# Optimization experiments

Measured on AMD Instinct MI355X. Metric: run time of the kernel, lower is better.

## Reference

```python
import jax, jax.numpy as jnp
import numpy as np
import math

B, S, IN_DIM = 4, 2048, 256
ATT_DIM, NUM_HEADS, TOP_K = 128, 4, 32


def _linear_params(key, out_dim, in_dim):
    kw, kb = jax.random.split(key)
    bound = 1.0 / math.sqrt(in_dim)
    w = jax.random.uniform(kw, (out_dim, in_dim), jnp.float32, -bound, bound)
    b = jax.random.uniform(kb, (out_dim,), jnp.float32, -bound, bound)
    return w, b


def setup_inputs() -> dict:
    key = jax.random.key(0)
    keys = jax.random.split(key, 16)
    x = jax.random.normal(keys[0], (B, S, IN_DIM), jnp.float32)
    tp_w, tp_b = _linear_params(keys[1], ATT_DIM, IN_DIM)
    sp_w, sp_b = _linear_params(keys[2], ATT_DIM, IN_DIM)
    ta_qw, ta_qb = _linear_params(keys[3], ATT_DIM, ATT_DIM)
    ta_kw, ta_kb = _linear_params(keys[4], ATT_DIM, ATT_DIM)
    ta_vw, ta_vb = _linear_params(keys[5], ATT_DIM, ATT_DIM)
    ta_ow, ta_ob = _linear_params(keys[6], ATT_DIM, ATT_DIM)
    sa_qw, sa_qb = _linear_params(keys[7], ATT_DIM, ATT_DIM)
    sa_kw, sa_kb = _linear_params(keys[8], ATT_DIM, ATT_DIM)
    sa_vw, sa_vb = _linear_params(keys[9], ATT_DIM, ATT_DIM)
    sa_ow, sa_ob = _linear_params(keys[10], ATT_DIM, ATT_DIM)
    gate_w, gate_b = _linear_params(keys[11], ATT_DIM, 2 * ATT_DIM)
    fus_w, fus_b = _linear_params(keys[12], ATT_DIM, 2 * ATT_DIM)
    return dict(x=x, tp_w=tp_w, tp_b=tp_b, sp_w=sp_w, sp_b=sp_b,
                ta_qw=ta_qw, ta_qb=ta_qb, ta_kw=ta_kw, ta_kb=ta_kb,
                ta_vw=ta_vw, ta_vb=ta_vb, ta_ow=ta_ow, ta_ob=ta_ob,
                sa_qw=sa_qw, sa_qb=sa_qb, sa_kw=sa_kw, sa_kb=sa_kb,
                sa_vw=sa_vw, sa_vb=sa_vb, sa_ow=sa_ow, sa_ob=sa_ob,
                gate_w=gate_w, gate_b=gate_b, fus_w=fus_w, fus_b=fus_b)


def _lin(x, w, b):
    return x @ w.T + b


def _sparse_topk_attention(x, qw, qb, kw, kb, vw, vb, ow, ob):
    # x: [B, S, E]; dropout is identity in eval mode
    b, s, e = x.shape
    h, d = NUM_HEADS, e // NUM_HEADS
    q = _lin(x, qw, qb).reshape(b, s, h, d).transpose(0, 2, 1, 3)  # [B,H,S,D]
    k = _lin(x, kw, kb).reshape(b, s, h, d).transpose(0, 2, 1, 3)
    v = _lin(x, vw, vb).reshape(b, s, h, d).transpose(0, 2, 1, 3)
    scores = jnp.einsum('bhqd,bhkd->bhqk', q, k) / math.sqrt(d)  # [B,H,S,S]
    kk = min(TOP_K, s)
    top_scores, top_idx = jax.lax.top_k(scores, kk)  # [B,H,S,K]
    soft = jax.nn.softmax(top_scores, axis=-1)
    # scatter softmaxed top-k weights into a zero [B,H,S,S] matrix (faithful to source)
    bi = jnp.arange(b)[:, None, None, None]
    hi = jnp.arange(h)[None, :, None, None]
    si = jnp.arange(s)[None, None, :, None]
    sparse = jnp.zeros_like(scores).at[bi, hi, si, top_idx].set(soft)
    out = jnp.einsum('bhqk,bhkd->bhqd', sparse, v)
    out = out.transpose(0, 2, 1, 3).reshape(b, s, e)
    return _lin(out, ow, ob)


def reference(x, tp_w, tp_b, sp_w, sp_b,
              ta_qw, ta_qb, ta_kw, ta_kb, ta_vw, ta_vb, ta_ow, ta_ob,
              sa_qw, sa_qb, sa_kw, sa_kb, sa_vw, sa_vb, sa_ow, sa_ob,
              gate_w, gate_b, fus_w, fus_b):
    temporal = _lin(x, tp_w, tp_b)
    temporal = _sparse_topk_attention(temporal, ta_qw, ta_qb, ta_kw, ta_kb,
                                      ta_vw, ta_vb, ta_ow, ta_ob)
    semantic = _lin(x, sp_w, sp_b)
    semantic = _sparse_topk_attention(semantic, sa_qw, sa_qb, sa_kw, sa_kb,
                                      sa_vw, sa_vb, sa_ow, sa_ob)
    concat = jnp.concatenate([temporal, semantic], axis=-1)  # [B,S,2A]
    gate = jax.nn.sigmoid(_lin(concat, gate_w, gate_b))
    fused = _lin(concat, fus_w, fus_b) * gate
    return fused
```

## Files before the change

### kernel.cpp

```cpp
#include <hip/hip_runtime.h>
#include <math.h>

#define B_   4
#define S_   2048
#define AD   128
#define NH   4
#define HD   32
#define TK   32
#define SEG  1048576
#define CAP  192

#define OFF_PROJ 0
#define OFF_Q    (1 * SEG)
#define OFF_K    (2 * SEG)
#define OFF_V    (3 * SEG)
#define OFF_ATT  (4 * SEG)
#define OFF_T    (5 * SEG)
#define OFF_SB   (6 * SEG)
#define OFF_CAT  (7 * SEG)

__device__ float g_ws[9 * SEG];
__device__ float g_sc[8 * S_ * S_];

__device__ __forceinline__ unsigned f2key(float s) {
    unsigned u = __float_as_uint(s);
    return (u & 0x80000000u) ? ~u : (u | 0x80000000u);
}
__device__ __forceinline__ float key2f(unsigned k) {
    unsigned u = (k & 0x80000000u) ? (k & 0x7FFFFFFFu) : ~k;
    return __uint_as_float(u);
}

template <int KD>
__global__ __launch_bounds__(256)
void lin_kernel(const float* __restrict__ Xext, int xoff,
                const float* __restrict__ W, const float* __restrict__ Bv,
                int yoff)
{
    const float* X = Xext ? Xext : (const float*)(g_ws + xoff);
    float* Y = g_ws + yoff;
    __shared__ float Xs[32][68];
    __shared__ float Ws[32][68];
    const int bm = blockIdx.x * 64;
    const int bn = blockIdx.y * 64;
    const int t  = threadIdx.x;
    const int tx = t & 15, ty = t >> 4;
    const int sr = t >> 3, sc4 = t & 7;
    float acc[4][4] = {};
    for (int kk = 0; kk < KD; kk += 32) {
        #pragma unroll
        for (int it = 0; it < 2; ++it) {
            int rr = sr + it * 32;
            float4 xa = *(const float4*)(X + (size_t)(bm + rr) * KD + kk + sc4 * 4);
            float4 wa = *(const float4*)(W + (size_t)(bn + rr) * KD + kk + sc4 * 4);
            Xs[sc4*4+0][rr] = xa.x; Xs[sc4*4+1][rr] = xa.y;
            Xs[sc4*4+2][rr] = xa.z; Xs[sc4*4+3][rr] = xa.w;
            Ws[sc4*4+0][rr] = wa.x; Ws[sc4*4+1][rr] = wa.y;
            Ws[sc4*4+2][rr] = wa.z; Ws[sc4*4+3][rr] = wa.w;
        }
        __syncthreads();
        #pragma unroll
        for (int kc = 0; kc < 32; ++kc) {
            float4 a4 = *(const float4*)&Xs[kc][ty * 4];
            float4 b4 = *(const float4*)&Ws[kc][tx * 4];
            float a[4] = {a4.x, a4.y, a4.z, a4.w};
            float bb[4] = {b4.x, b4.y, b4.z, b4.w};
            #pragma unroll
            for (int i = 0; i < 4; ++i)
                #pragma unroll
                for (int j = 0; j < 4; ++j)
                    acc[i][j] = fmaf(a[i], bb[j], acc[i][j]);
        }
        __syncthreads();
    }
    #pragma unroll
    for (int i = 0; i < 4; ++i) {
        int row = bm + ty * 4 + i;
        int col = bn + tx * 4;
        float4 o;
        o.x = acc[i][0] + Bv[col + 0]; o.y = acc[i][1] + Bv[col + 1];
        o.z = acc[i][2] + Bv[col + 2]; o.w = acc[i][3] + Bv[col + 3];
        *(float4*)(Y + (size_t)row * AD + col) = o;
    }
}

template <int KD>
__global__ __launch_bounds__(256)
void lin3_kernel(int xoff,
                 const float* __restrict__ W0, const float* __restrict__ B0, int y0,
                 const float* __restrict__ W1, const float* __restrict__ B1, int y1,
                 const float* __restrict__ W2, const float* __restrict__ B2, int y2)
{
    const int z = blockIdx.z;
    const float* X = (const float*)(g_ws + xoff);
    const float* W = (z == 0) ? W0 : (z == 1) ? W1 : W2;
    const float* Bv = (z == 0) ? B0 : (z == 1) ? B1 : B2;
    float* Y = g_ws + ((z == 0) ? y0 : (z == 1) ? y1 : y2);
    __shared__ float Xs[32][68];
    __shared__ float Ws[32][68];
    const int bm = blockIdx.x * 64;
    const int bn = blockIdx.y * 64;
    const int t  = threadIdx.x;
    const int tx = t & 15, ty = t >> 4;
    const int sr = t >> 3, sc4 = t & 7;
    float acc[4][4] = {};
    for (int kk = 0; kk < KD; kk += 32) {
        #pragma unroll
        for (int it = 0; it < 2; ++it) {
            int rr = sr + it * 32;
            float4 xa = *(const float4*)(X + (size_t)(bm + rr) * KD + kk + sc4 * 4);
            float4 wa = *(const float4*)(W + (size_t)(bn + rr) * KD + kk + sc4 * 4);
            Xs[sc4*4+0][rr] = xa.x; Xs[sc4*4+1][rr] = xa.y;
            Xs[sc4*4+2][rr] = xa.z; Xs[sc4*4+3][rr] = xa.w;
            Ws[sc4*4+0][rr] = wa.x; Ws[sc4*4+1][rr] = wa.y;
            Ws[sc4*4+2][rr] = wa.z; Ws[sc4*4+3][rr] = wa.w;
        }
        __syncthreads();
        #pragma unroll
        for (int kc = 0; kc < 32; ++kc) {
            float4 a4 = *(const float4*)&Xs[kc][ty * 4];
            float4 b4 = *(const float4*)&Ws[kc][tx * 4];
            float a[4] = {a4.x, a4.y, a4.z, a4.w};
            float bb[4] = {b4.x, b4.y, b4.z, b4.w};
            #pragma unroll
            for (int i = 0; i < 4; ++i)
                #pragma unroll
                for (int j = 0; j < 4; ++j)
                    acc[i][j] = fmaf(a[i], bb[j], acc[i][j]);
        }
        __syncthreads();
    }
    #pragma unroll
    for (int i = 0; i < 4; ++i) {
        int row = bm + ty * 4 + i;
        int col = bn + tx * 4;
        float4 o;
        o.x = acc[i][0] + Bv[col + 0]; o.y = acc[i][1] + Bv[col + 1];
        o.z = acc[i][2] + Bv[col + 2]; o.w = acc[i][3] + Bv[col + 3];
        *(float4*)(Y + (size_t)row * AD + col) = o;
    }
}

__global__ __launch_bounds__(256)
void score_kernel(int qoff, int koff, int chunk)
{
    const int zh = blockIdx.z;
    const int hh = chunk * 8 + zh, b = hh >> 2, h = hh & 3;
    const float* Qb = g_ws + qoff + (size_t)b * S_ * AD + h * HD;
    const float* Kb = g_ws + koff + (size_t)b * S_ * AD + h * HD;
    float* Sc = g_sc + (size_t)zh * S_ * S_;
    __shared__ float Qs[32][68];
    __shared__ float Ks[32][68];
    const int t = threadIdx.x, tx = t & 15, ty = t >> 4;
    const int sr = t >> 3, sc4 = t & 7;
    const int q0 = blockIdx.y * 64, k0 = blockIdx.x * 64;
    #pragma unroll
    for (int it = 0; it < 2; ++it) {
        int rr = sr + it * 32;
        float4 qa = *(const float4*)(Qb + (size_t)(q0 + rr) * AD + sc4 * 4);
        float4 ka = *(const float4*)(Kb + (size_t)(k0 + rr) * AD + sc4 * 4);
        Qs[sc4*4+0][rr] = qa.x; Qs[sc4*4+1][rr] = qa.y;
        Qs[sc4*4+2][rr] = qa.z; Qs[sc4*4+3][rr] = qa.w;
        Ks[sc4*4+0][rr] = ka.x; Ks[sc4*4+1][rr] = ka.y;
        Ks[sc4*4+2][rr] = ka.z; Ks[sc4*4+3][rr] = ka.w;
    }
    __syncthreads();
    float acc[4][4] = {};
    #pragma unroll
    for (int kc = 0; kc < 32; ++kc) {
        float4 a4 = *(const float4*)&Qs[kc][ty * 4];
        float4 b4 = *(const float4*)&Ks[kc][tx * 4];
        float a[4] = {a4.x, a4.y, a4.z, a4.w};
        float bb[4] = {b4.x, b4.y, b4.z, b4.w};
        #pragma unroll
        for (int i = 0; i < 4; ++i)
            #pragma unroll
            for (int j = 0; j < 4; ++j)
                acc[i][j] = fmaf(a[i], bb[j], acc[i][j]);
    }
    const float scale = 0.17677669529663688f;
    #pragma unroll
    for (int i = 0; i < 4; ++i) {
        float4 o;
        o.x = acc[i][0] * scale; o.y = acc[i][1] * scale;
        o.z = acc[i][2] * scale; o.w = acc[i][3] * scale;
        *(float4*)(Sc + (size_t)(q0 + ty * 4 + i) * S_ + k0 + tx * 4) = o;
    }
}

__global__ __launch_bounds__(256)
void topk_kernel(int voff, int ooff, int chunk)
{
    const float* V = g_ws + voff;
    float* O = g_ws + ooff;

    __shared__ unsigned long long sve[4][CAP];
    __shared__ float    wsel[4][32];
    __shared__ unsigned jsel[4][32];

    const int wid  = threadIdx.x >> 6;
    const int lane = threadIdx.x & 63;
    const int gr   = blockIdx.x * 4 + wid;
    const int zh   = gr >> 11, q = gr & 2047;
    const int hh   = chunk * 8 + zh;
    const int b    = hh >> 2,  h = hh & 3;

    unsigned long long* sv = sve[wid];
    float*    wp = wsel[wid];
    unsigned* jp = jsel[wid];

    const float* Srow  = g_sc + (size_t)zh * S_ * S_ + (size_t)q * S_;
    const float* vbase = V + (size_t)b * S_ * AD + h * HD;

    float4 s4[8];
    #pragma unroll
    for (int i = 0; i < 8; ++i) s4[i] = ((const float4*)Srow)[i * 64 + lane];
    unsigned keys[32];
    unsigned lmax = 0u;
    #pragma unroll
    for (int i = 0; i < 8; ++i) {
        unsigned k0 = f2key(s4[i].x), k1 = f2key(s4[i].y);
        unsigned k2 = f2key(s4[i].z), k3 = f2key(s4[i].w);
        keys[i * 4 + 0] = k0; keys[i * 4 + 1] = k1;
        keys[i * 4 + 2] = k2; keys[i * 4 + 3] = k3;
        unsigned m01 = (k0 > k1) ? k0 : k1;
        unsigned m23 = (k2 > k3) ? k2 : k3;
        unsigned m = (m01 > m23) ? m01 : m23;
        lmax = (m > lmax) ? m : lmax;
    }

    unsigned bs = lmax;
    #pragma unroll
    for (int k = 2; k <= 64; k <<= 1) {
        #pragma unroll
        for (int j = k >> 1; j > 0; j >>= 1) {
            unsigned o = (unsigned)__shfl_xor((int)bs, j);
            bool up = ((lane & k) == 0);
            bool lower = ((lane & j) == 0);
            bs = (up == lower) ? (bs < o ? bs : o) : (bs > o ? bs : o);
        }
    }
    const unsigned thr  = (unsigned)__shfl((int)bs, 32);
    const unsigned mkey = (unsigned)__shfl((int)bs, 63);
    const float Mf = key2f(mkey);

    int base = 0;
    const unsigned long long lt = (1ull << lane) - 1ull;
    #pragma unroll
    for (int t = 0; t < 32; ++t) {
        bool pred = keys[t] >= thr;
        unsigned long long m = __ballot(pred);
        int slot = base + __popcll(m & lt);
        if (pred && slot < CAP) {
            unsigned jidx = (unsigned)((t >> 2) * 256 + lane * 4 + (t & 3));
            sv[slot] = ((unsigned long long)keys[t] << 32) | (unsigned)(2047 - jidx);
        }
        base += __popcll(m);
    }
    const int S = base;
    asm volatile("s_waitcnt lgkmcnt(0)" ::: "memory");

    if (S <= 64) {
        unsigned long long pi = (lane < S) ? sv[lane] : 0ull;
        int rank = 0;
        for (int jx = 0; jx < S; ++jx)
            rank += (sv[jx] > pi) ? 1 : 0;
        float e = 0.f; unsigned ji = 0;
        if (lane < S && rank < TK) {
            float val = key2f((unsigned)(pi >> 32));
            e = __expf(val - Mf);
            ji = 2047u - (unsigned)(pi & 0xFFFFFFFFull);
        }
        float esum = e;
        #pragma unroll
        for (int off = 1; off < 64; off <<= 1) esum += __shfl_xor(esum, off);
        if (lane < S && rank < TK) { wp[rank] = e / esum; jp[rank] = ji; }
    } else if (S <= CAP) {
        unsigned long long pi[3]; int rk[3]; float ee[3]; unsigned jj[3];
        float esum = 0.f;
        #pragma unroll
        for (int u = 0; u < 3; ++u) {
            int i = lane + u * 64;
            pi[u] = (i < S) ? sv[i] : 0ull;
            rk[u] = 0; ee[u] = 0.f; jj[u] = 0;
        }
        for (int jx = 0; jx < S; ++jx) {
            unsigned long long pj = sv[jx];
            #pragma unroll
            for (int u = 0; u < 3; ++u)
                rk[u] += (pj > pi[u]) ? 1 : 0;
        }
        #pragma unroll
        for (int u = 0; u < 3; ++u) {
            int i = lane + u * 64;
            if (i < S && rk[u] < TK) {
                float val = key2f((unsigned)(pi[u] >> 32));
                ee[u] = __expf(val - Mf);
                jj[u] = 2047u - (unsigned)(pi[u] & 0xFFFFFFFFull);
                esum += ee[u];
            }
        }
        #pragma unroll
        for (int off = 1; off < 64; off <<= 1) esum += __shfl_xor(esum, off);
        #pragma unroll
        for (int u = 0; u < 3; ++u) {
            int i = lane + u * 64;
            if (i < S && rk[u] < TK) { wp[rk[u]] = ee[u] / esum; jp[rk[u]] = jj[u]; }
        }
    } else {
        unsigned consumed = 0u;
        for (int i = 0; i < TK; ++i) {
            unsigned bk = 0u; unsigned gj = 0xFFFFFFFFu;
            #pragma unroll
            for (int t = 0; t < 32; ++t) {
                if (((consumed >> t) & 1u) == 0u) {
                    unsigned kk = keys[t];
                    unsigned j = (unsigned)((t >> 2) * 256 + lane * 4 + (t & 3));
                    if (kk > bk || (kk == bk && j < gj)) { bk = kk; gj = j; }
                }
            }
            #pragma unroll
            for (int off = 1; off < 64; off <<= 1) {
                unsigned ok = (unsigned)__shfl_xor((int)bk, off);
                unsigned oj = (unsigned)__shfl_xor((int)gj, off);
                if (ok > bk || (ok == bk && oj < gj)) { bk = ok; gj = oj; }
            }
            if (((gj >> 2) & 63u) == (unsigned)lane && gj != 0xFFFFFFFFu) {
                int t = ((int)gj >> 8) * 4 + ((int)gj & 3);
                consumed |= (1u << t);
            }
            if (lane == 0) { wp[i] = key2f(bk); jp[i] = gj; }
        }
        asm volatile("s_waitcnt lgkmcnt(0)" ::: "memory");
        float v = (lane < TK) ? wp[lane] : 0.f;
        float e = (lane < TK) ? __expf(v - Mf) : 0.f;
        float esum = e;
        #pragma unroll
        for (int off = 1; off < 64; off <<= 1) esum += __shfl_xor(esum, off);
        if (lane < TK) wp[lane] = e / esum;
    }
    asm volatile("s_waitcnt lgkmcnt(0)" ::: "memory");

    float oacc = 0.f;
    const int dd = lane & 31, half = lane >> 5;
    #pragma unroll
    for (int u2 = 0; u2 < 16; ++u2) {
        int i = half * 16 + u2;
        oacc = fmaf(wp[i], vbase[(size_t)jp[i] * AD + dd], oacc);
    }
    oacc += __shfl_down(oacc, 32);
    if (lane < HD) O[((size_t)b * S_ + q) * AD + h * HD + lane] = oacc;
}

__global__ __launch_bounds__(256)
void concat_kernel()
{
    int i = blockIdx.x * 256 + threadIdx.x;
    int row = i >> 8, c = i & 255;
    float v = (c < AD) ? g_ws[OFF_T + row * AD + c]
                       : g_ws[OFF_SB + row * AD + (c - AD)];
    g_ws[OFF_CAT + i] = v;
}

__global__ __launch_bounds__(256)
void fuse_kernel(float* __restrict__ out)
{
    int i = blockIdx.x * 256 + threadIdx.x;
    float g = g_ws[OFF_Q + i];
    float f = g_ws[OFF_K + i];
    out[i] = f / (1.0f + expf(-g));
}

extern "C" void kernel_launch(void* const* d_in, const int* in_sizes, int n_in,
                              void* d_out, int out_size, void* d_ws, size_t ws_size,
                              hipStream_t stream)
{
    (void)in_sizes; (void)n_in; (void)d_ws; (void)ws_size; (void)out_size;
    const float* x      = (const float*)d_in[0];
    const float* tp_w   = (const float*)d_in[1];
    const float* tp_b   = (const float*)d_in[2];
    const float* sp_w   = (const float*)d_in[3];
    const float* sp_b   = (const float*)d_in[4];
    const float* gate_w = (const float*)d_in[21];
    const float* gate_b = (const float*)d_in[22];
    const float* fus_w  = (const float*)d_in[23];
    const float* fus_b  = (const float*)d_in[24];

    dim3 gl(128, 2);
    for (int br = 0; br < 2; ++br) {
        const float* pw = br ? sp_w : tp_w;
        const float* pb = br ? sp_b : tp_b;
        int base = 5 + br * 8;
        const float* qw = (const float*)d_in[base + 0];
        const float* qb = (const float*)d_in[base + 1];
        const float* kw = (const float*)d_in[base + 2];
        const float* kb = (const float*)d_in[base + 3];
        const float* vw = (const float*)d_in[base + 4];
        const float* vb = (const float*)d_in[base + 5];
        const float* ow = (const float*)d_in[base + 6];
        const float* ob = (const float*)d_in[base + 7];

        lin_kernel<256><<<gl, 256, 0, stream>>>(x, 0, pw, pb, OFF_PROJ);
        lin3_kernel<128><<<dim3(128, 2, 3), 256, 0, stream>>>(
            OFF_PROJ, qw, qb, OFF_Q, kw, kb, OFF_K, vw, vb, OFF_V);
        for (int chunk = 0; chunk < 2; ++chunk) {
            score_kernel<<<dim3(32, 32, 8), 256, 0, stream>>>(OFF_Q, OFF_K, chunk);
            topk_kernel<<<4096, 256, 0, stream>>>(OFF_V, OFF_ATT, chunk);
        }
        lin_kernel<128><<<gl, 256, 0, stream>>>(nullptr, OFF_ATT, ow, ob,
                                                br ? OFF_SB : OFF_T);
    }
    concat_kernel<<<8192, 256, 0, stream>>>();
    lin3_kernel<256><<<dim3(128, 2, 2), 256, 0, stream>>>(
        OFF_CAT, gate_w, gate_b, OFF_Q, fus_w, fus_b, OFF_K,
        (const float*)nullptr, (const float*)nullptr, 0);
    fuse_kernel<<<4096, 256, 0, stream>>>((float*)d_out);
}
```

Measured before the change: 373.3 us.

## Store 16-bit score keys and recompute exact scores for top-k candidates

The score kernel now writes only the upper 16 bits of the order-preserving key instead of full fp32 scores. That halves the size of the score matrix, so all 16 heads fit in one buffer and the per-chunk launch loop can be dropped. The top-k kernel filters candidates with the truncated keys, then recomputes exact fp32 dot products from Q and K for those candidates before ranking and the softmax. This trades score-matrix memory traffic for extra gathered K reads. The fallback path, used when there are too many candidates, recomputes all 2048 scores per row.

```diff
diff --git a/kernel.cpp b/kernel.cpp
--- a/kernel.cpp
+++ b/kernel.cpp
@@ -20,7 +20,7 @@
 #define OFF_CAT  (7 * SEG)
 
 __device__ float g_ws[9 * SEG];
-__device__ float g_sc[8 * S_ * S_];
+__device__ unsigned short g_sp[16 * S_ * S_];
 
 __device__ __forceinline__ unsigned f2key(float s) {
     unsigned u = __float_as_uint(s);
@@ -142,13 +142,12 @@
 }
 
 __global__ __launch_bounds__(256)
-void score_kernel(int qoff, int koff, int chunk)
-{
-    const int zh = blockIdx.z;
-    const int hh = chunk * 8 + zh, b = hh >> 2, h = hh & 3;
+void score_kernel(int qoff, int koff)
+{
+    const int hh = blockIdx.z, b = hh >> 2, h = hh & 3;
     const float* Qb = g_ws + qoff + (size_t)b * S_ * AD + h * HD;
     const float* Kb = g_ws + koff + (size_t)b * S_ * AD + h * HD;
-    float* Sc = g_sc + (size_t)zh * S_ * S_;
+    unsigned short* Sc = g_sp + (size_t)hh * S_ * S_;
     __shared__ float Qs[32][68];
     __shared__ float Ks[32][68];
     const int t = threadIdx.x, tx = t & 15, ty = t >> 4;
@@ -181,19 +180,19 @@
     const float scale = 0.17677669529663688f;
     #pragma unroll
     for (int i = 0; i < 4; ++i) {
-        float4 o;
-        o.x = acc[i][0] * scale; o.y = acc[i][1] * scale;
-        o.z = acc[i][2] * scale; o.w = acc[i][3] * scale;
-        *(float4*)(Sc + (size_t)(q0 + ty * 4 + i) * S_ + k0 + tx * 4) = o;
-    }
-}
-
-__global__ __launch_bounds__(256)
-void topk_kernel(int voff, int ooff, int chunk)
-{
-    const float* V = g_ws + voff;
-    float* O = g_ws + ooff;
-
+        ushort4 o;
+        o.x = (unsigned short)(f2key(acc[i][0] * scale) >> 16);
+        o.y = (unsigned short)(f2key(acc[i][1] * scale) >> 16);
+        o.z = (unsigned short)(f2key(acc[i][2] * scale) >> 16);
+        o.w = (unsigned short)(f2key(acc[i][3] * scale) >> 16);
+        *(ushort4*)(Sc + (size_t)(q0 + ty * 4 + i) * S_ + k0 + tx * 4) = o;
+    }
+}
+
+__global__ __launch_bounds__(256)
+void topk_kernel(int qoff, int koff, int voff, int ooff)
+{
+    __shared__ unsigned cnd[4][CAP];
     __shared__ unsigned long long sve[4][CAP];
     __shared__ float    wsel[4][32];
     __shared__ unsigned jsel[4][32];
@@ -201,31 +200,32 @@
     const int wid  = threadIdx.x >> 6;
     const int lane = threadIdx.x & 63;
     const int gr   = blockIdx.x * 4 + wid;
-    const int zh   = gr >> 11, q = gr & 2047;
-    const int hh   = chunk * 8 + zh;
+    const int hh   = gr >> 11, q = gr & 2047;
     const int b    = hh >> 2,  h = hh & 3;
 
+    unsigned* cp = cnd[wid];
     unsigned long long* sv = sve[wid];
     float*    wp = wsel[wid];
     unsigned* jp = jsel[wid];
 
-    const float* Srow  = g_sc + (size_t)zh * S_ * S_ + (size_t)q * S_;
-    const float* vbase = V + (size_t)b * S_ * AD + h * HD;
-
-    float4 s4[8];
-    #pragma unroll
-    for (int i = 0; i < 8; ++i) s4[i] = ((const float4*)Srow)[i * 64 + lane];
-    unsigned keys[32];
+    const unsigned short* Prow = g_sp + (size_t)hh * S_ * S_ + (size_t)q * S_;
+    const float* qrow  = g_ws + qoff + ((size_t)b * S_ + q) * AD + h * HD;
+    const float* kbase = g_ws + koff + (size_t)b * S_ * AD + h * HD;
+    const float* vbase = g_ws + voff + (size_t)b * S_ * AD + h * HD;
+    float* O = g_ws + ooff;
+    const float scale = 0.17677669529663688f;
+
+    unsigned pwv[16];
     unsigned lmax = 0u;
     #pragma unroll
-    for (int i = 0; i < 8; ++i) {
-        unsigned k0 = f2key(s4[i].x), k1 = f2key(s4[i].y);
-        unsigned k2 = f2key(s4[i].z), k3 = f2key(s4[i].w);
-        keys[i * 4 + 0] = k0; keys[i * 4 + 1] = k1;
-        keys[i * 4 + 2] = k2; keys[i * 4 + 3] = k3;
-        unsigned m01 = (k0 > k1) ? k0 : k1;
-        unsigned m23 = (k2 > k3) ? k2 : k3;
-        unsigned m = (m01 > m23) ? m01 : m23;
+    for (int i = 0; i < 4; ++i) {
+        uint4 u = ((const uint4*)Prow)[i * 64 + lane];
+        pwv[i*4+0] = u.x; pwv[i*4+1] = u.y; pwv[i*4+2] = u.z; pwv[i*4+3] = u.w;
+    }
+    #pragma unroll
+    for (int w = 0; w < 16; ++w) {
+        unsigned lo = pwv[w] & 0xFFFFu, hi = pwv[w] >> 16;
+        unsigned m = (lo > hi) ? lo : hi;
         lmax = (m > lmax) ? m : lmax;
     }
 
@@ -235,87 +235,138 @@
         #pragma unroll
         for (int j = k >> 1; j > 0; j >>= 1) {
             unsigned o = (unsigned)__shfl_xor((int)bs, j);
-            bool up = ((lane & k) == 0);
-            bool lower = ((lane & j) == 0);
-            bs = (up == lower) ? (bs < o ? bs : o) : (bs > o ? bs : o);
-        }
-    }
-    const unsigned thr  = (unsigned)__shfl((int)bs, 32);
-    const unsigned mkey = (unsigned)__shfl((int)bs, 63);
-    const float Mf = key2f(mkey);
-
-    int base = 0;
+            bool keepmin = (((lane & k) == 0) == ((lane & j) == 0));
+            bs = keepmin ? (bs < o ? bs : o) : (bs > o ? bs : o);
+        }
+    }
+    const unsigned t16 = (unsigned)__shfl((int)bs, 32);
+
+    asm volatile("s_waitcnt lgkmcnt(0)" ::: "memory");
+    int S = 0;
     const unsigned long long lt = (1ull << lane) - 1ull;
     #pragma unroll
-    for (int t = 0; t < 32; ++t) {
-        bool pred = keys[t] >= thr;
-        unsigned long long m = __ballot(pred);
-        int slot = base + __popcll(m & lt);
-        if (pred && slot < CAP) {
-            unsigned jidx = (unsigned)((t >> 2) * 256 + lane * 4 + (t & 3));
-            sv[slot] = ((unsigned long long)keys[t] << 32) | (unsigned)(2047 - jidx);
-        }
-        base += __popcll(m);
-    }
-    const int S = base;
+    for (int i = 0; i < 4; ++i)
+        #pragma unroll
+        for (int j = 0; j < 4; ++j)
+            #pragma unroll
+            for (int hf = 0; hf < 2; ++hf) {
+                unsigned w = pwv[i*4+j];
+                unsigned p = hf ? (w >> 16) : (w & 0xFFFFu);
+                bool pred = p >= t16;
+                unsigned long long m = __ballot(pred);
+                int slot = S + __popcll(m & lt);
+                if (pred && slot < CAP)
+                    cp[slot] = (unsigned)(512*i + 8*lane + 2*j + hf);
+                S += __popcll(m);
+            }
     asm volatile("s_waitcnt lgkmcnt(0)" ::: "memory");
 
-    if (S <= 64) {
-        unsigned long long pi = (lane < S) ? sv[lane] : 0ull;
-        int rank = 0;
-        for (int jx = 0; jx < S; ++jx)
-            rank += (sv[jx] > pi) ? 1 : 0;
-        float e = 0.f; unsigned ji = 0;
-        if (lane < S && rank < TK) {
-            float val = key2f((unsigned)(pi >> 32));
-            e = __expf(val - Mf);
-            ji = 2047u - (unsigned)(pi & 0xFFFFFFFFull);
-        }
-        float esum = e;
-        #pragma unroll
-        for (int off = 1; off < 64; off <<= 1) esum += __shfl_xor(esum, off);
-        if (lane < S && rank < TK) { wp[rank] = e / esum; jp[rank] = ji; }
-    } else if (S <= CAP) {
-        unsigned long long pi[3]; int rk[3]; float ee[3]; unsigned jj[3];
-        float esum = 0.f;
+    float qv[32];
+    #pragma unroll
+    for (int g = 0; g < 8; ++g) {
+        float4 t4 = ((const float4*)qrow)[g];
+        qv[g*4+0] = t4.x; qv[g*4+1] = t4.y; qv[g*4+2] = t4.z; qv[g*4+3] = t4.w;
+    }
+
+    if (S <= CAP) {
+        unsigned long long pk[3];
         #pragma unroll
         for (int u = 0; u < 3; ++u) {
             int i = lane + u * 64;
-            pi[u] = (i < S) ? sv[i] : 0ull;
-            rk[u] = 0; ee[u] = 0.f; jj[u] = 0;
-        }
-        for (int jx = 0; jx < S; ++jx) {
-            unsigned long long pj = sv[jx];
-            #pragma unroll
-            for (int u = 0; u < 3; ++u)
-                rk[u] += (pj > pi[u]) ? 1 : 0;
-        }
-        #pragma unroll
-        for (int u = 0; u < 3; ++u) {
-            int i = lane + u * 64;
-            if (i < S && rk[u] < TK) {
-                float val = key2f((unsigned)(pi[u] >> 32));
-                ee[u] = __expf(val - Mf);
-                jj[u] = 2047u - (unsigned)(pi[u] & 0xFFFFFFFFull);
-                esum += ee[u];
-            }
-        }
-        #pragma unroll
-        for (int off = 1; off < 64; off <<= 1) esum += __shfl_xor(esum, off);
-        #pragma unroll
-        for (int u = 0; u < 3; ++u) {
-            int i = lane + u * 64;
-            if (i < S && rk[u] < TK) { wp[rk[u]] = ee[u] / esum; jp[rk[u]] = jj[u]; }
+            pk[u] = 0ull;
+            if (i < S) {
+                unsigned ji = cp[i];
+                const float4* kp = (const float4*)(kbase + (size_t)ji * AD);
+                float s = 0.f;
+                #pragma unroll
+                for (int g = 0; g < 8; ++g) {
+                    float4 kv = kp[g];
+                    s = fmaf(qv[g*4+0], kv.x, s); s = fmaf(qv[g*4+1], kv.y, s);
+                    s = fmaf(qv[g*4+2], kv.z, s); s = fmaf(qv[g*4+3], kv.w, s);
+                }
+                unsigned key = f2key(s * scale);
+                pk[u] = ((unsigned long long)key << 32) | (unsigned)(2047 - ji);
+                sv[i] = pk[u];
+            }
+        }
+        asm volatile("s_waitcnt lgkmcnt(0)" ::: "memory");
+
+        unsigned long long mk = pk[0];
+        mk = (pk[1] > mk) ? pk[1] : mk;
+        mk = (pk[2] > mk) ? pk[2] : mk;
+        #pragma unroll
+        for (int off = 1; off < 64; off <<= 1) {
+            unsigned long long o =
+                (unsigned long long)__shfl_xor((long long)mk, off);
+            mk = (o > mk) ? o : mk;
+        }
+        const float Mf = key2f((unsigned)(mk >> 32));
+
+        if (S <= 64) {
+            unsigned long long pi = pk[0];
+            int rank = 0;
+            for (int jx = 0; jx < S; ++jx)
+                rank += (sv[jx] > pi) ? 1 : 0;
+            float e = 0.f; unsigned ji = 0;
+            if (lane < S && rank < TK) {
+                e = __expf(key2f((unsigned)(pi >> 32)) - Mf);
+                ji = 2047u - (unsigned)(pi & 0xFFFFFFFFull);
+            }
+            float esum = e;
+            #pragma unroll
+            for (int off = 1; off < 64; off <<= 1) esum += __shfl_xor(esum, off);
+            if (lane < S && rank < TK) { wp[rank] = e / esum; jp[rank] = ji; }
+        } else {
+            int rk[3]; float ee[3]; unsigned jj[3];
+            float esum = 0.f;
+            #pragma unroll
+            for (int u = 0; u < 3; ++u) { rk[u] = 0; ee[u] = 0.f; jj[u] = 0; }
+            for (int jx = 0; jx < S; ++jx) {
+                unsigned long long pj = sv[jx];
+                #pragma unroll
+                for (int u = 0; u < 3; ++u)
+                    rk[u] += (pj > pk[u]) ? 1 : 0;
+            }
+            #pragma unroll
+            for (int u = 0; u < 3; ++u) {
+                int i = lane + u * 64;
+                if (i < S && rk[u] < TK) {
+                    ee[u] = __expf(key2f((unsigned)(pk[u] >> 32)) - Mf);
+                    jj[u] = 2047u - (unsigned)(pk[u] & 0xFFFFFFFFull);
+                    esum += ee[u];
+                }
+            }
+            #pragma unroll
+            for (int off = 1; off < 64; off <<= 1) esum += __shfl_xor(esum, off);
+            #pragma unroll
+            for (int u = 0; u < 3; ++u) {
+                int i = lane + u * 64;
+                if (i < S && rk[u] < TK) { wp[rk[u]] = ee[u] / esum; jp[rk[u]] = jj[u]; }
+            }
         }
     } else {
+        unsigned keys[32];
+        #pragma unroll
+        for (int t = 0; t < 32; ++t) {
+            const float4* kp = (const float4*)(kbase + (size_t)(t * 64 + lane) * AD);
+            float s = 0.f;
+            #pragma unroll
+            for (int g = 0; g < 8; ++g) {
+                float4 kv = kp[g];
+                s = fmaf(qv[g*4+0], kv.x, s); s = fmaf(qv[g*4+1], kv.y, s);
+                s = fmaf(qv[g*4+2], kv.z, s); s = fmaf(qv[g*4+3], kv.w, s);
+            }
+            keys[t] = f2key(s * scale);
+        }
         unsigned consumed = 0u;
+        unsigned mfk = 0u;
         for (int i = 0; i < TK; ++i) {
             unsigned bk = 0u; unsigned gj = 0xFFFFFFFFu;
             #pragma unroll
             for (int t = 0; t < 32; ++t) {
                 if (((consumed >> t) & 1u) == 0u) {
                     unsigned kk = keys[t];
-                    unsigned j = (unsigned)((t >> 2) * 256 + lane * 4 + (t & 3));
+                    unsigned j = (unsigned)(t * 64 + lane);
                     if (kk > bk || (kk == bk && j < gj)) { bk = kk; gj = j; }
                 }
             }
@@ -325,13 +376,13 @@
                 unsigned oj = (unsigned)__shfl_xor((int)gj, off);
                 if (ok > bk || (ok == bk && oj < gj)) { bk = ok; gj = oj; }
             }
-            if (((gj >> 2) & 63u) == (unsigned)lane && gj != 0xFFFFFFFFu) {
-                int t = ((int)gj >> 8) * 4 + ((int)gj & 3);
-                consumed |= (1u << t);
-            }
+            if (i == 0) mfk = bk;
+            if ((gj & 63u) == (unsigned)lane && gj != 0xFFFFFFFFu)
+                consumed |= (1u << (gj >> 6));
             if (lane == 0) { wp[i] = key2f(bk); jp[i] = gj; }
         }
         asm volatile("s_waitcnt lgkmcnt(0)" ::: "memory");
+        const float Mf = key2f(mfk);
         float v = (lane < TK) ? wp[lane] : 0.f;
         float e = (lane < TK) ? __expf(v - Mf) : 0.f;
         float esum = e;
@@ -403,10 +454,8 @@
         lin_kernel<256><<<gl, 256, 0, stream>>>(x, 0, pw, pb, OFF_PROJ);
         lin3_kernel<128><<<dim3(128, 2, 3), 256, 0, stream>>>(
             OFF_PROJ, qw, qb, OFF_Q, kw, kb, OFF_K, vw, vb, OFF_V);
-        for (int chunk = 0; chunk < 2; ++chunk) {
-            score_kernel<<<dim3(32, 32, 8), 256, 0, stream>>>(OFF_Q, OFF_K, chunk);
-            topk_kernel<<<4096, 256, 0, stream>>>(OFF_V, OFF_ATT, chunk);
-        }
+        score_kernel<<<dim3(32, 32, 16), 256, 0, stream>>>(OFF_Q, OFF_K);
+        topk_kernel<<<8192, 256, 0, stream>>>(OFF_Q, OFF_K, OFF_V, OFF_ATT);
         lin_kernel<128><<<gl, 256, 0, stream>>>(nullptr, OFF_ATT, ow, ob,
                                                 br ? OFF_SB : OFF_T);
     }
```

Measured after the change: 447.0 us. +19.7%, slower.
